# Kernel tuning notes

Measured on AMD Instinct MI355X. Metric: run time of the kernel, lower is better.

Reference implementation:

```python
import jax, jax.numpy as jnp
import numpy as np


def setup_inputs() -> dict:
    key = jax.random.key(0)
    x = jax.random.normal(key, (4, 4096, 384), dtype=jnp.float32)
    return {"x": x}


def reference(x):
    # x: [B, T, 3C] -> q, k, v each [B, T, C]
    csz = x.shape[-1]
    c = csz // 3
    q, k, v = x[..., :c], x[..., c:2 * c], x[..., 2 * c:]
    # NOTE: original computes k @ q^T (not q @ k^T)
    scale = 1.0 / np.sqrt(c).astype(np.float32)
    score = jnp.einsum('btc,bsc->bts', k, q) * scale  # [B, T, T]
    kernel = jax.nn.softmax(score, axis=-1)
    out = jnp.einsum('bts,bsc->btc', kernel, v)  # [B, T, C]
    return out
```

## Files before the change

### kernel.cpp

```cpp
#include <hip/hip_runtime.h>
#include <hip/hip_bf16.h>

typedef __bf16 bf16x8 __attribute__((ext_vector_type(8)));
typedef __bf16 bf16x4 __attribute__((ext_vector_type(4)));
typedef float  f32x4  __attribute__((ext_vector_type(4)));

#define NROW 4096
#define XSTR 384
#define DHEAD 128
#define QBLK 64
#define KVB 128
#define NIT (NROW / KVB)

__launch_bounds__(512, 2)
__global__ void attn_fwd_kernel(const float* __restrict__ x, float* __restrict__ out) {
    const int b   = blockIdx.y;
    const int t0  = blockIdx.x * QBLK;
    const int tid = threadIdx.x;
    const int w   = tid >> 6;
    const int wq  = w & 3;
    const int kvh = w >> 2;
    const int l   = tid & 63;
    const int lr  = l & 15;
    const int lg  = l >> 4;

    __shared__ union {
        struct { __bf16 Kt[128][132]; __bf16 Vt[128][132]; } t;
        struct { float O[4][16][128]; float m[4][16]; float lsum[4][16]; } mrg;
    } U;
    __shared__ __bf16 Pl[8][16][68];

    const float* xb = x + (size_t)b * NROW * XSTR;

    bf16x8 qf[4];
    {
        const float* qrow = xb + (size_t)(t0 + wq * 16 + lr) * XSTR + DHEAD;
        #pragma unroll
        for (int kc = 0; kc < 4; ++kc) {
            const float4 f0 = *(const float4*)(qrow + kc * 32 + lg * 8);
            const float4 f1 = *(const float4*)(qrow + kc * 32 + lg * 8 + 4);
            bf16x8 v;
            v[0] = (__bf16)f0.x; v[1] = (__bf16)f0.y; v[2] = (__bf16)f0.z; v[3] = (__bf16)f0.w;
            v[4] = (__bf16)f1.x; v[5] = (__bf16)f1.y; v[6] = (__bf16)f1.z; v[7] = (__bf16)f1.w;
            qf[kc] = v;
        }
    }

    f32x4 oacc[8];
    #pragma unroll
    for (int i = 0; i < 8; ++i) { f32x4 z = {0.f, 0.f, 0.f, 0.f}; oacc[i] = z; }
    float mrow[4], lrow[4];
    #pragma unroll
    for (int r = 0; r < 4; ++r) { mrow[r] = -1e30f; lrow[r] = 0.f; }

    const float C = 0.08838834764831845f * 1.44269504088896340f;

    const int krow = tid >> 5;
    const int kcol = (tid & 31) << 2;

    float4 pk[8], pv[8];

    auto prefetch = [&](int S0) {
        #pragma unroll
        for (int i = 0; i < 8; ++i)
            pk[i] = *(const float4*)(xb + (size_t)(S0 + krow + i * 16) * XSTR + kcol);
        #pragma unroll
        for (int i2 = 0; i2 < 2; ++i2) {
            const int cb = (krow + i2 * 16) << 2;
            #pragma unroll
            for (int r = 0; r < 4; ++r)
                pv[i2 * 4 + r] = *(const float4*)(xb + (size_t)(S0 + kcol + r) * XSTR + 256 + cb);
        }
    };
    auto write_lds = [&]() {
        #pragma unroll
        for (int i = 0; i < 8; ++i) {
            const float* f = (const float*)&pk[i];
            bf16x4 v;
            v[0] = (__bf16)f[0]; v[1] = (__bf16)f[1]; v[2] = (__bf16)f[2]; v[3] = (__bf16)f[3];
            *(bf16x4*)&U.t.Kt[krow + i * 16][kcol] = v;
        }
        #pragma unroll
        for (int i2 = 0; i2 < 2; ++i2) {
            const int cb = (krow + i2 * 16) << 2;
            #pragma unroll
            for (int cc = 0; cc < 4; ++cc) {
                bf16x4 v;
                #pragma unroll
                for (int r = 0; r < 4; ++r)
                    v[r] = (__bf16)((const float*)&pv[i2 * 4 + r])[cc];
                *(bf16x4*)&U.t.Vt[cb + cc][kcol] = v;
            }
        }
    };

    prefetch(0);
    write_lds();
    __syncthreads();

    for (int it = 0; it < NIT; ++it) {
        if (it + 1 < NIT) prefetch((it + 1) * KVB);

        const int sb = kvh * 64;

        f32x4 sacc[4];
        #pragma unroll
        for (int st = 0; st < 4; ++st) { f32x4 z = {0.f, 0.f, 0.f, 0.f}; sacc[st] = z; }
        #pragma unroll
        for (int kc = 0; kc < 4; ++kc) {
            #pragma unroll
            for (int st = 0; st < 4; ++st) {
                bf16x8 bf = *(const bf16x8*)&U.t.Kt[sb + st * 16 + lr][kc * 32 + lg * 8];
                sacc[st] = __builtin_amdgcn_mfma_f32_16x16x32_bf16(qf[kc], bf, sacc[st], 0, 0, 0);
            }
        }

        float rmax[4], psum[4], alpha[4];
        #pragma unroll
        for (int r = 0; r < 4; ++r)
            rmax[r] = fmaxf(fmaxf(sacc[0][r], sacc[1][r]), fmaxf(sacc[2][r], sacc[3][r]));
        #pragma unroll
        for (int mk = 1; mk <= 8; mk <<= 1) {
            #pragma unroll
            for (int r = 0; r < 4; ++r) rmax[r] = fmaxf(rmax[r], __shfl_xor(rmax[r], mk));
        }
        #pragma unroll
        for (int r = 0; r < 4; ++r) {
            float mnew = fmaxf(mrow[r], rmax[r]);
            alpha[r]   = __builtin_amdgcn_exp2f((mrow[r] - mnew) * C);
            mrow[r]    = mnew;
            psum[r]    = 0.f;
        }
        #pragma unroll
        for (int st = 0; st < 4; ++st) {
            #pragma unroll
            for (int r = 0; r < 4; ++r) {
                float p = __builtin_amdgcn_exp2f((sacc[st][r] - mrow[r]) * C);
                psum[r] += p;
                Pl[w][lg * 4 + r][st * 16 + lr] = (__bf16)p;
            }
        }
        #pragma unroll
        for (int mk = 1; mk <= 8; mk <<= 1) {
            #pragma unroll
            for (int r = 0; r < 4; ++r) psum[r] += __shfl_xor(psum[r], mk);
        }
        #pragma unroll
        for (int r = 0; r < 4; ++r) lrow[r] = lrow[r] * alpha[r] + psum[r];
        #pragma unroll
        for (int ct = 0; ct < 8; ++ct) {
            #pragma unroll
            for (int r = 0; r < 4; ++r) oacc[ct][r] *= alpha[r];
        }

        bf16x8 pa0 = *(const bf16x8*)&Pl[w][lr][lg * 8];
        bf16x8 pa1 = *(const bf16x8*)&Pl[w][lr][32 + lg * 8];
        #pragma unroll
        for (int ct = 0; ct < 8; ++ct) {
            bf16x8 b0 = *(const bf16x8*)&U.t.Vt[ct * 16 + lr][sb + lg * 8];
            bf16x8 b1 = *(const bf16x8*)&U.t.Vt[ct * 16 + lr][sb + 32 + lg * 8];
            oacc[ct] = __builtin_amdgcn_mfma_f32_16x16x32_bf16(pa0, b0, oacc[ct], 0, 0, 0);
            oacc[ct] = __builtin_amdgcn_mfma_f32_16x16x32_bf16(pa1, b1, oacc[ct], 0, 0, 0);
        }
        __syncthreads();
        if (it + 1 < NIT) { write_lds(); __syncthreads(); }
    }

    if (kvh == 1) {
        #pragma unroll
        for (int ct = 0; ct < 8; ++ct) {
            #pragma unroll
            for (int r = 0; r < 4; ++r)
                U.mrg.O[wq][lg * 4 + r][ct * 16 + lr] = oacc[ct][r];
        }
        if (lr == 0) {
            #pragma unroll
            for (int r = 0; r < 4; ++r) {
                U.mrg.m[wq][lg * 4 + r]    = mrow[r];
                U.mrg.lsum[wq][lg * 4 + r] = lrow[r];
            }
        }
    }
    __syncthreads();
    if (kvh == 0) {
        float* orow = out + ((size_t)b * NROW + t0 + wq * 16) * DHEAD;
        #pragma unroll
        for (int r = 0; r < 4; ++r) {
            const float m2 = U.mrg.m[wq][lg * 4 + r];
            const float l2 = U.mrg.lsum[wq][lg * 4 + r];
            const float mm = fmaxf(mrow[r], m2);
            const float a1 = __builtin_amdgcn_exp2f((mrow[r] - mm) * C);
            const float a2 = __builtin_amdgcn_exp2f((m2 - mm) * C);
            const float inv = 1.f / (lrow[r] * a1 + l2 * a2);
            #pragma unroll
            for (int ct = 0; ct < 8; ++ct) {
                const float o2 = U.mrg.O[wq][lg * 4 + r][ct * 16 + lr];
                orow[(size_t)(lg * 4 + r) * DHEAD + ct * 16 + lr] =
                    (oacc[ct][r] * a1 + o2 * a2) * inv;
            }
        }
    }
}

extern "C" void kernel_launch(void* const* d_in, const int* in_sizes, int n_in,
                              void* d_out, int out_size, void* d_ws, size_t ws_size,
                              hipStream_t stream) {
    const float* x = (const float*)d_in[0];
    float* out = (float*)d_out;
    dim3 grid(NROW / QBLK, 4);
    attn_fwd_kernel<<<grid, 512, 0, stream>>>(x, out);
}
```

Measured before the change: 212.4 us.

## Halve query tile, split KV four ways, swizzle blocks across XCDs

Reduces the query block to 32 rows so twice as many workgroups launch. Each workgroup now has 2 query warps and 4 KV-partition warps merged with a 4-way online-softmax combine. The grid is remapped so consecutive blocks land on the same XCD for L2 reuse, and setprio is raised around the MFMA loops. The aim is higher occupancy and better latency hiding, but every block still loads full K/V, so global/L2 traffic for K/V doubles.

After: 581.2 us. 174% more time.

```diff
diff --git a/kernel.cpp b/kernel.cpp
--- a/kernel.cpp
+++ b/kernel.cpp
@@ -8,27 +8,31 @@
 #define NROW 4096
 #define XSTR 384
 #define DHEAD 128
-#define QBLK 64
+#define QBLK 32
 #define KVB 128
 #define NIT (NROW / KVB)
 
-__launch_bounds__(512, 2)
+__launch_bounds__(512, 4)
 __global__ void attn_fwd_kernel(const float* __restrict__ x, float* __restrict__ out) {
-    const int b   = blockIdx.y;
-    const int t0  = blockIdx.x * QBLK;
+    const int bid  = blockIdx.x;
+    const int orig = (bid & 7) * 64 + (bid >> 3);
+    const int b    = orig >> 7;
+    const int t0   = (orig & 127) * QBLK;
+
     const int tid = threadIdx.x;
     const int w   = tid >> 6;
-    const int wq  = w & 3;
-    const int kvh = w >> 2;
+    const int wq  = w & 1;
+    const int kvq = w >> 1;
     const int l   = tid & 63;
     const int lr  = l & 15;
     const int lg  = l >> 4;
+    const int sq  = kvq * 32;
 
     __shared__ union {
-        struct { __bf16 Kt[128][132]; __bf16 Vt[128][132]; } t;
-        struct { float O[4][16][128]; float m[4][16]; float lsum[4][16]; } mrg;
+        struct { __bf16 Kt[KVB][136]; __bf16 Vt[DHEAD][136]; } t;
+        struct { float O[3][2][16][132]; float m[3][2][16]; float lsum[3][2][16]; } mrg;
     } U;
-    __shared__ __bf16 Pl[8][16][68];
+    __shared__ __bf16 Pl[8][16][40];
 
     const float* xb = x + (size_t)b * NROW * XSTR;
 
@@ -101,24 +105,23 @@
     for (int it = 0; it < NIT; ++it) {
         if (it + 1 < NIT) prefetch((it + 1) * KVB);
 
-        const int sb = kvh * 64;
-
-        f32x4 sacc[4];
-        #pragma unroll
-        for (int st = 0; st < 4; ++st) { f32x4 z = {0.f, 0.f, 0.f, 0.f}; sacc[st] = z; }
+        f32x4 sacc[2];
+        #pragma unroll
+        for (int st = 0; st < 2; ++st) { f32x4 z = {0.f, 0.f, 0.f, 0.f}; sacc[st] = z; }
+        __builtin_amdgcn_s_setprio(1);
         #pragma unroll
         for (int kc = 0; kc < 4; ++kc) {
             #pragma unroll
-            for (int st = 0; st < 4; ++st) {
-                bf16x8 bf = *(const bf16x8*)&U.t.Kt[sb + st * 16 + lr][kc * 32 + lg * 8];
+            for (int st = 0; st < 2; ++st) {
+                bf16x8 bf = *(const bf16x8*)&U.t.Kt[sq + st * 16 + lr][kc * 32 + lg * 8];
                 sacc[st] = __builtin_amdgcn_mfma_f32_16x16x32_bf16(qf[kc], bf, sacc[st], 0, 0, 0);
             }
         }
+        __builtin_amdgcn_s_setprio(0);
 
         float rmax[4], psum[4], alpha[4];
         #pragma unroll
-        for (int r = 0; r < 4; ++r)
-            rmax[r] = fmaxf(fmaxf(sacc[0][r], sacc[1][r]), fmaxf(sacc[2][r], sacc[3][r]));
+        for (int r = 0; r < 4; ++r) rmax[r] = fmaxf(sacc[0][r], sacc[1][r]);
         #pragma unroll
         for (int mk = 1; mk <= 8; mk <<= 1) {
             #pragma unroll
@@ -132,7 +135,7 @@
             psum[r]    = 0.f;
         }
         #pragma unroll
-        for (int st = 0; st < 4; ++st) {
+        for (int st = 0; st < 2; ++st) {
             #pragma unroll
             for (int r = 0; r < 4; ++r) {
                 float p = __builtin_amdgcn_exp2f((sacc[st][r] - mrow[r]) * C);
@@ -153,50 +156,62 @@
             for (int r = 0; r < 4; ++r) oacc[ct][r] *= alpha[r];
         }
 
-        bf16x8 pa0 = *(const bf16x8*)&Pl[w][lr][lg * 8];
-        bf16x8 pa1 = *(const bf16x8*)&Pl[w][lr][32 + lg * 8];
+        bf16x8 pa = *(const bf16x8*)&Pl[w][lr][lg * 8];
+        __builtin_amdgcn_s_setprio(1);
         #pragma unroll
         for (int ct = 0; ct < 8; ++ct) {
-            bf16x8 b0 = *(const bf16x8*)&U.t.Vt[ct * 16 + lr][sb + lg * 8];
-            bf16x8 b1 = *(const bf16x8*)&U.t.Vt[ct * 16 + lr][sb + 32 + lg * 8];
-            oacc[ct] = __builtin_amdgcn_mfma_f32_16x16x32_bf16(pa0, b0, oacc[ct], 0, 0, 0);
-            oacc[ct] = __builtin_amdgcn_mfma_f32_16x16x32_bf16(pa1, b1, oacc[ct], 0, 0, 0);
-        }
+            bf16x8 bv = *(const bf16x8*)&U.t.Vt[ct * 16 + lr][sq + lg * 8];
+            oacc[ct] = __builtin_amdgcn_mfma_f32_16x16x32_bf16(pa, bv, oacc[ct], 0, 0, 0);
+        }
+        __builtin_amdgcn_s_setprio(0);
+
         __syncthreads();
         if (it + 1 < NIT) { write_lds(); __syncthreads(); }
     }
 
-    if (kvh == 1) {
+    if (kvq > 0) {
         #pragma unroll
         for (int ct = 0; ct < 8; ++ct) {
             #pragma unroll
             for (int r = 0; r < 4; ++r)
-                U.mrg.O[wq][lg * 4 + r][ct * 16 + lr] = oacc[ct][r];
+                U.mrg.O[kvq - 1][wq][lg * 4 + r][ct * 16 + lr] = oacc[ct][r];
         }
         if (lr == 0) {
             #pragma unroll
             for (int r = 0; r < 4; ++r) {
-                U.mrg.m[wq][lg * 4 + r]    = mrow[r];
-                U.mrg.lsum[wq][lg * 4 + r] = lrow[r];
+                U.mrg.m[kvq - 1][wq][lg * 4 + r]    = mrow[r];
+                U.mrg.lsum[kvq - 1][wq][lg * 4 + r] = lrow[r];
             }
         }
     }
     __syncthreads();
-    if (kvh == 0) {
+    if (kvq == 0) {
         float* orow = out + ((size_t)b * NROW + t0 + wq * 16) * DHEAD;
         #pragma unroll
         for (int r = 0; r < 4; ++r) {
-            const float m2 = U.mrg.m[wq][lg * 4 + r];
-            const float l2 = U.mrg.lsum[wq][lg * 4 + r];
-            const float mm = fmaxf(mrow[r], m2);
-            const float a1 = __builtin_amdgcn_exp2f((mrow[r] - mm) * C);
-            const float a2 = __builtin_amdgcn_exp2f((m2 - mm) * C);
-            const float inv = 1.f / (lrow[r] * a1 + l2 * a2);
+            float mp[3], lp[3];
+            #pragma unroll
+            for (int p = 0; p < 3; ++p) {
+                mp[p] = U.mrg.m[p][wq][lg * 4 + r];
+                lp[p] = U.mrg.lsum[p][wq][lg * 4 + r];
+            }
+            float mm = fmaxf(fmaxf(mrow[r], mp[0]), fmaxf(mp[1], mp[2]));
+            const float a0 = __builtin_amdgcn_exp2f((mrow[r] - mm) * C);
+            float ap[3];
+            float denom = lrow[r] * a0;
+            #pragma unroll
+            for (int p = 0; p < 3; ++p) {
+                ap[p] = __builtin_amdgcn_exp2f((mp[p] - mm) * C);
+                denom += lp[p] * ap[p];
+            }
+            const float inv = 1.f / denom;
             #pragma unroll
             for (int ct = 0; ct < 8; ++ct) {
-                const float o2 = U.mrg.O[wq][lg * 4 + r][ct * 16 + lr];
-                orow[(size_t)(lg * 4 + r) * DHEAD + ct * 16 + lr] =
-                    (oacc[ct][r] * a1 + o2 * a2) * inv;
+                float o = oacc[ct][r] * a0;
+                #pragma unroll
+                for (int p = 0; p < 3; ++p)
+                    o += U.mrg.O[p][wq][lg * 4 + r][ct * 16 + lr] * ap[p];
+                orow[(size_t)(lg * 4 + r) * DHEAD + ct * 16 + lr] = o * inv;
             }
         }
     }
@@ -207,6 +222,5 @@
                               hipStream_t stream) {
     const float* x = (const float*)d_in[0];
     float* out = (float*)d_out;
-    dim3 grid(NROW / QBLK, 4);
-    attn_fwd_kernel<<<grid, 512, 0, stream>>>(x, out);
+    attn_fwd_kernel<<<dim3(512), 512, 0, stream>>>(x, out);
 }
```
